# Performance work log

Measured on AMD Instinct MI355X. Metric: run time of the kernel, lower is better.

The kernel has to match this reference:

```python
import jax, jax.numpy as jnp
import numpy as np

D_MODEL = 1024
N_HEAD = 16
B, T = 4, 2048


def setup_inputs() -> dict:
    key = jax.random.key(0)
    k1, k2, k3, k4, k5 = jax.random.split(key, 5)
    s = 0.02
    return {
        "x": jax.random.normal(k1, (B, T, D_MODEL), dtype=jnp.float32),
        "w_attn": jax.random.normal(k2, (3 * D_MODEL, D_MODEL), dtype=jnp.float32) * s,
        "b_attn": jax.random.normal(k3, (3 * D_MODEL,), dtype=jnp.float32) * s,
        "w_proj": jax.random.normal(k4, (D_MODEL, D_MODEL), dtype=jnp.float32) * s,
        "b_proj": jax.random.normal(k5, (D_MODEL,), dtype=jnp.float32) * s,
    }


def reference(x, w_attn, b_attn, w_proj, b_proj):
    # x: [B, T, C]
    Bb, Tt, C = x.shape
    H = N_HEAD
    dk = C // H
    scale = 1.0 / np.sqrt(dk).astype(np.float32)

    qkv = x @ w_attn.T + b_attn                      # [B, T, 3C]
    q, k, v = jnp.split(qkv, 3, axis=-1)             # each [B, T, C]
    # -> [B, H, T, dk]
    q = q.reshape(Bb, Tt, H, dk).transpose(0, 2, 1, 3)
    k = k.reshape(Bb, Tt, H, dk).transpose(0, 2, 1, 3)
    v = v.reshape(Bb, Tt, H, dk).transpose(0, 2, 1, 3)

    att = jnp.einsum("bhqd,bhkd->bhqk", q, k) * scale   # [B, H, T, T]
    att = jax.nn.softmax(att, axis=-1)
    y = jnp.einsum("bhqk,bhkd->bhqd", att, v)            # [B, H, T, dk]
    y = y.transpose(0, 2, 1, 3).reshape(Bb, Tt, C)       # [B, T, C]
    return y @ w_proj.T + b_proj
```

## Files before the change

kernel.cpp:

```cpp
#include <hip/hip_runtime.h>
#include <hip/hip_bf16.h>

typedef __attribute__((ext_vector_type(8))) short short8;
typedef __attribute__((ext_vector_type(4))) short short4v;
typedef __attribute__((ext_vector_type(4))) float floatx4;
typedef __attribute__((ext_vector_type(16))) float floatx16;

#define B_ 4
#define T_ 2048
#define C_ 1024
#define H_ 16
#define DK_ 64
#define M_ (B_ * T_)
#define N3_ (3 * C_)

#define QSCALE 0.1803368801111243f

__device__ __forceinline__ unsigned short f2bf(float f) {
    union { float f; unsigned u; } v; v.f = f;
    unsigned r = v.u + 0x7fffu + ((v.u >> 16) & 1u);
    return (unsigned short)(r >> 16);
}
__device__ __forceinline__ unsigned fbits(float f) {
    union { float f; unsigned u; } v; v.f = f; return v.u;
}
__device__ __forceinline__ unsigned pack_bf16(float a, float b) {
#if __has_builtin(__builtin_amdgcn_cvt_pk_bf16_f32)
    typedef __attribute__((ext_vector_type(2))) __bf16 bf16x2;
    bf16x2 r = __builtin_amdgcn_cvt_pk_bf16_f32(a, b);
    union { bf16x2 v; unsigned u; } c; c.v = r; return c.u;
#else
    return __builtin_amdgcn_perm(fbits(b) + 0x8000u, fbits(a) + 0x8000u, 0x07060302u);
#endif
}

__device__ __forceinline__ void gload_lds16(const unsigned short* g, unsigned short* l) {
    __builtin_amdgcn_global_load_lds(
        (const __attribute__((address_space(1))) unsigned int*)(const void*)g,
        (__attribute__((address_space(3))) unsigned int*)(void*)l, 16, 0, 0);
}

#define NX4 (M_ * C_ / 4)
#define NA4 (N3_ * C_ / 4)
#define NP4 (C_ * C_ / 4)
__global__ __launch_bounds__(256) void cast3_kernel(const float* __restrict__ x,
                                                    const float* __restrict__ wa,
                                                    const float* __restrict__ wp,
                                                    unsigned short* __restrict__ xb,
                                                    unsigned short* __restrict__ wab,
                                                    unsigned short* __restrict__ wpb) {
    int i = blockIdx.x * 256 + threadIdx.x;
    const float* src; unsigned short* dst; int j;
    if (i < NX4) { src = x; dst = xb; j = i; }
    else if (i < NX4 + NA4) { src = wa; dst = wab; j = i - NX4; }
    else { src = wp; dst = wpb; j = i - NX4 - NA4; }
    float4 v = ((const float4*)src)[j];
    ushort4 o;
    o.x = f2bf(v.x); o.y = f2bf(v.y); o.z = f2bf(v.z); o.w = f2bf(v.w);
    ((ushort4*)dst)[j] = o;
}

#define BM 128
#define BN 128
#define BK 32

__global__ __launch_bounds__(256) void gemm_qkv(const unsigned short* __restrict__ A,
                                                const unsigned short* __restrict__ W,
                                                const float* __restrict__ bias,
                                                unsigned short* __restrict__ qout,
                                                unsigned short* __restrict__ kout,
                                                unsigned short* __restrict__ vout) {
    const int Kd = C_;
    __shared__ unsigned short As[BM * BK];
    __shared__ unsigned short Bs[BN * BK];
    int lin = blockIdx.y * gridDim.x + blockIdx.x;
    int cpx = (gridDim.x * gridDim.y) >> 3;
    int swz = (lin & 7) * cpx + (lin >> 3);
    int m0 = (swz / gridDim.x) * BM;
    int n0 = (swz % gridDim.x) * BN;
    int tid = threadIdx.x;
    int lane = tid & 63, w = tid >> 6;
    int wm = (w >> 1) * 64, wn = (w & 1) * 64;
    int l16 = lane & 15, quad = lane >> 4;
    int r4 = lane >> 2, c4 = (lane & 3) * 8;

    floatx4 acc[4][4] = {};
    for (int kt = 0; kt < Kd; kt += BK) {
        __syncthreads();
        for (int t = 0; t < 2; ++t) {
            int rbase = w * 32 + t * 16;
            gload_lds16(&A[(size_t)(m0 + rbase + r4) * Kd + kt + c4], &As[rbase * BK]);
            gload_lds16(&W[(size_t)(n0 + rbase + r4) * Kd + kt + c4], &Bs[rbase * BK]);
        }
        __syncthreads();
        short8 af[4], bf[4];
        for (int i = 0; i < 4; ++i)
            af[i] = *(const short8*)&As[(wm + 16 * i + l16) * BK + quad * 8];
        for (int j = 0; j < 4; ++j)
            bf[j] = *(const short8*)&Bs[(wn + 16 * j + l16) * BK + quad * 8];
        for (int i = 0; i < 4; ++i)
            for (int j = 0; j < 4; ++j)
                acc[i][j] = __builtin_amdgcn_mfma_f32_16x16x32_bf16(af[i], bf[j], acc[i][j], 0, 0, 0);
    }
    for (int i = 0; i < 4; ++i)
        for (int j = 0; j < 4; ++j) {
            int col = n0 + wn + 16 * j + l16;
            float bval = bias[col];
            int sec = col >> 10, cc = col & 1023;
            int h = cc >> 6, d = cc & 63;
            float qs = (sec == 0) ? QSCALE : 1.0f;
            unsigned short* dst = (sec == 0) ? qout : ((sec == 1) ? kout : vout);
            for (int r = 0; r < 4; ++r) {
                int m = m0 + wm + 16 * i + quad * 4 + r;
                int b = m >> 11, t = m & (T_ - 1);
                int bh = b * H_ + h;
                dst[((size_t)bh * T_ + t) * DK_ + d] = f2bf((acc[i][j][r] + bval) * qs);
            }
        }
}

__global__ __launch_bounds__(256) void gemm_proj(const unsigned short* __restrict__ A,
                                                 const unsigned short* __restrict__ W,
                                                 const float* __restrict__ bias,
                                                 float* __restrict__ out) {
    const int Kd = C_;
    __shared__ unsigned short As[BM * BK];
    __shared__ unsigned short Bs[BN * BK];
    int lin = blockIdx.y * gridDim.x + blockIdx.x;
    int cpx = (gridDim.x * gridDim.y) >> 3;
    int swz = (lin & 7) * cpx + (lin >> 3);
    int m0 = (swz / gridDim.x) * BM;
    int n0 = (swz % gridDim.x) * BN;
    int tid = threadIdx.x;
    int lane = tid & 63, w = tid >> 6;
    int wm = (w >> 1) * 64, wn = (w & 1) * 64;
    int l16 = lane & 15, quad = lane >> 4;
    int r4 = lane >> 2, c4 = (lane & 3) * 8;

    floatx4 acc[4][4] = {};
    for (int kt = 0; kt < Kd; kt += BK) {
        __syncthreads();
        for (int t = 0; t < 2; ++t) {
            int rbase = w * 32 + t * 16;
            gload_lds16(&A[(size_t)(m0 + rbase + r4) * Kd + kt + c4], &As[rbase * BK]);
            gload_lds16(&W[(size_t)(n0 + rbase + r4) * Kd + kt + c4], &Bs[rbase * BK]);
        }
        __syncthreads();
        short8 af[4], bf[4];
        for (int i = 0; i < 4; ++i)
            af[i] = *(const short8*)&As[(wm + 16 * i + l16) * BK + quad * 8];
        for (int j = 0; j < 4; ++j)
            bf[j] = *(const short8*)&Bs[(wn + 16 * j + l16) * BK + quad * 8];
        for (int i = 0; i < 4; ++i)
            for (int j = 0; j < 4; ++j)
                acc[i][j] = __builtin_amdgcn_mfma_f32_16x16x32_bf16(af[i], bf[j], acc[i][j], 0, 0, 0);
    }
    for (int i = 0; i < 4; ++i)
        for (int j = 0; j < 4; ++j) {
            int col = n0 + wn + 16 * j + l16;
            float bval = bias[col];
            for (int r = 0; r < 4; ++r) {
                int m = m0 + wm + 16 * i + quad * 4 + r;
                out[(size_t)m * C_ + col] = acc[i][j][r] + bval;
            }
        }
}

#define TLD 258
__global__ __launch_bounds__(256) void vtrans_kernel(const unsigned short* __restrict__ V,
                                                     unsigned short* __restrict__ Vt) {
    __shared__ unsigned short L[64 * TLD];
    int bid = blockIdx.x;
    int t0 = (bid & 7) * 256;
    int bh = bid >> 3;
    int tid = threadIdx.x;
    const unsigned short* src = V + ((size_t)bh * T_ + t0) * DK_;
    unsigned short* dst = Vt + (size_t)bh * DK_ * T_ + t0;
    for (int it = 0; it < 8; ++it) {
        int t = it * 32 + (tid >> 3);
        int dseg = (tid & 7) * 8;
        short8 v = *(const short8*)&src[(size_t)t * DK_ + dseg];
        for (int j = 0; j < 8; ++j)
            L[(dseg + j) * TLD + t] = ((unsigned short*)&v)[j];
    }
    __syncthreads();
    for (int it = 0; it < 8; ++it) {
        int d = it * 8 + (tid >> 5);
        int toff = (tid & 31) * 8;
        short8 r = *(const short8*)&L[d * TLD + toff];
        *(short8*)&dst[(size_t)d * T_ + toff] = r;
    }
}

#define KT 64
#define LD 72

__global__ __launch_bounds__(256, 2) void attn_kernel(const unsigned short* __restrict__ Q,
                                                      const unsigned short* __restrict__ Kv,
                                                      const unsigned short* __restrict__ Vt,
                                                      unsigned short* __restrict__ Y) {
    __shared__ unsigned short smem[128 * LD];
    unsigned short* Ks = smem;
    unsigned short* Vts = smem + 64 * LD;

    int bid = blockIdx.x;
    int qt = bid & 7;
    int bh = bid >> 3;
    int b = bh >> 4, hh = bh & 15;
    const unsigned short* qh = Q + (size_t)bh * T_ * DK_;
    const unsigned short* kh = Kv + (size_t)bh * T_ * DK_;
    const unsigned short* vtg = Vt + (size_t)bh * DK_ * T_;

    int tid = threadIdx.x, lane = tid & 63, w = tid >> 6;
    int l31 = lane & 31, h = lane >> 5;
    int qrA = qt * 256 + w * 32;
    int qrB = qrA + 128;

    short8 qfA[4], qfB[4];
    for (int c = 0; c < 4; ++c) {
        qfA[c] = *(const short8*)&qh[(size_t)(qrA + l31) * DK_ + 16 * c + 8 * h];
        qfB[c] = *(const short8*)&qh[(size_t)(qrB + l31) * DK_ + 16 * c + 8 * h];
    }

    floatx16 oA0 = {}, oA1 = {}, oB0 = {}, oB1 = {};
    float lA = 0.f, lB = 0.f;

    for (int kt = 0; kt < T_; kt += KT) {
        __syncthreads();
        for (int it = 0; it < 2; ++it) {
            int idx = tid + it * 256;
            int r8 = idx >> 3, c8 = (idx & 7) * 8;
            *(short8*)&Ks[r8 * LD + c8] = *(const short8*)&kh[(size_t)(kt + r8) * DK_ + c8];
            int vd = r8 * LD + (c8 & 48) + ((c8 & 8) >> 1);
            union { short8 s; short4v q[2]; } u;
            u.s = *(const short8*)&vtg[(size_t)r8 * T_ + kt + c8];
            *(short4v*)&Vts[vd] = u.q[0];
            *(short4v*)&Vts[vd + 8] = u.q[1];
        }
        __syncthreads();

        floatx16 sA0 = {}, sA1 = {}, sB0 = {}, sB1 = {};
        for (int c = 0; c < 4; ++c) {
            short8 kf0 = *(const short8*)&Ks[l31 * LD + 16 * c + 8 * h];
            short8 kf1 = *(const short8*)&Ks[(32 + l31) * LD + 16 * c + 8 * h];
            sA0 = __builtin_amdgcn_mfma_f32_32x32x16_bf16(kf0, qfA[c], sA0, 0, 0, 0);
            sA1 = __builtin_amdgcn_mfma_f32_32x32x16_bf16(kf1, qfA[c], sA1, 0, 0, 0);
            sB0 = __builtin_amdgcn_mfma_f32_32x32x16_bf16(kf0, qfB[c], sB0, 0, 0, 0);
            sB1 = __builtin_amdgcn_mfma_f32_32x32x16_bf16(kf1, qfB[c], sB1, 0, 0, 0);
        }

        unsigned pA[16], pB[16];
        float tsA = 0.f, tsB = 0.f;
        for (int r2 = 0; r2 < 8; ++r2) {
            float a0 = __builtin_amdgcn_exp2f(sA0[2 * r2]);
            float a1 = __builtin_amdgcn_exp2f(sA0[2 * r2 + 1]);
            tsA += a0 + a1; pA[r2] = pack_bf16(a0, a1);
            float a2 = __builtin_amdgcn_exp2f(sA1[2 * r2]);
            float a3 = __builtin_amdgcn_exp2f(sA1[2 * r2 + 1]);
            tsA += a2 + a3; pA[8 + r2] = pack_bf16(a2, a3);
            float b0 = __builtin_amdgcn_exp2f(sB0[2 * r2]);
            float b1 = __builtin_amdgcn_exp2f(sB0[2 * r2 + 1]);
            tsB += b0 + b1; pB[r2] = pack_bf16(b0, b1);
            float b2 = __builtin_amdgcn_exp2f(sB1[2 * r2]);
            float b3 = __builtin_amdgcn_exp2f(sB1[2 * r2 + 1]);
            tsB += b2 + b3; pB[8 + r2] = pack_bf16(b2, b3);
        }
        lA += tsA; lB += tsB;

        for (int c = 0; c < 4; ++c) {
            short8 vf0 = *(const short8*)&Vts[l31 * LD + 16 * c + 8 * h];
            short8 vf1 = *(const short8*)&Vts[(32 + l31) * LD + 16 * c + 8 * h];
            union { unsigned u[4]; short8 s; } fA, fB;
            for (int j = 0; j < 4; ++j) { fA.u[j] = pA[4 * c + j]; fB.u[j] = pB[4 * c + j]; }
            oA0 = __builtin_amdgcn_mfma_f32_32x32x16_bf16(vf0, fA.s, oA0, 0, 0, 0);
            oA1 = __builtin_amdgcn_mfma_f32_32x32x16_bf16(vf1, fA.s, oA1, 0, 0, 0);
            oB0 = __builtin_amdgcn_mfma_f32_32x32x16_bf16(vf0, fB.s, oB0, 0, 0, 0);
            oB1 = __builtin_amdgcn_mfma_f32_32x32x16_bf16(vf1, fB.s, oB1, 0, 0, 0);
        }
    }

    float invA = 1.0f / (lA + __shfl_xor(lA, 32, 64));
    float invB = 1.0f / (lB + __shfl_xor(lB, 32, 64));
    int q_l = tid >> 1, seg = tid & 1;

    __syncthreads();
    for (int a = 0; a < 4; ++a) {
        ushort4 u;
        u.x = f2bf(oA0[4 * a + 0] * invA); u.y = f2bf(oA0[4 * a + 1] * invA);
        u.z = f2bf(oA0[4 * a + 2] * invA); u.w = f2bf(oA0[4 * a + 3] * invA);
        *(ushort4*)&smem[(w * 32 + l31) * LD + 8 * a + 4 * h] = u;
        ushort4 v;
        v.x = f2bf(oA1[4 * a + 0] * invA); v.y = f2bf(oA1[4 * a + 1] * invA);
        v.z = f2bf(oA1[4 * a + 2] * invA); v.w = f2bf(oA1[4 * a + 3] * invA);
        *(ushort4*)&smem[(w * 32 + l31) * LD + 32 + 8 * a + 4 * h] = v;
    }
    __syncthreads();
    {
        const unsigned short* srcp = &smem[(size_t)q_l * LD + seg * 32];
        unsigned short* dstp = &Y[((size_t)b * T_ + qt * 256 + q_l) * C_ + hh * DK_ + seg * 32];
        for (int j = 0; j < 4; ++j)
            *(short8*)&dstp[8 * j] = *(const short8*)&srcp[8 * j];
    }
    __syncthreads();
    for (int a = 0; a < 4; ++a) {
        ushort4 u;
        u.x = f2bf(oB0[4 * a + 0] * invB); u.y = f2bf(oB0[4 * a + 1] * invB);
        u.z = f2bf(oB0[4 * a + 2] * invB); u.w = f2bf(oB0[4 * a + 3] * invB);
        *(ushort4*)&smem[(w * 32 + l31) * LD + 8 * a + 4 * h] = u;
        ushort4 v;
        v.x = f2bf(oB1[4 * a + 0] * invB); v.y = f2bf(oB1[4 * a + 1] * invB);
        v.z = f2bf(oB1[4 * a + 2] * invB); v.w = f2bf(oB1[4 * a + 3] * invB);
        *(ushort4*)&smem[(w * 32 + l31) * LD + 32 + 8 * a + 4 * h] = v;
    }
    __syncthreads();
    {
        const unsigned short* srcp = &smem[(size_t)q_l * LD + seg * 32];
        unsigned short* dstp = &Y[((size_t)b * T_ + qt * 256 + 128 + q_l) * C_ + hh * DK_ + seg * 32];
        for (int j = 0; j < 4; ++j)
            *(short8*)&dstp[8 * j] = *(const short8*)&srcp[8 * j];
    }
}

extern "C" void kernel_launch(void* const* d_in, const int* in_sizes, int n_in,
                              void* d_out, int out_size, void* d_ws, size_t ws_size,
                              hipStream_t stream) {
    const float* x      = (const float*)d_in[0];
    const float* w_attn = (const float*)d_in[1];
    const float* b_attn = (const float*)d_in[2];
    const float* w_proj = (const float*)d_in[3];
    const float* b_proj = (const float*)d_in[4];
    float* out = (float*)d_out;

    unsigned short* ws = (unsigned short*)d_ws;
    unsigned short* xb  = ws;
    unsigned short* wab = xb  + (size_t)M_ * C_;
    unsigned short* wpb = wab + (size_t)N3_ * C_;
    unsigned short* qb  = wpb + (size_t)C_ * C_;
    unsigned short* kb  = qb  + (size_t)M_ * C_;
    unsigned short* vb  = kb  + (size_t)M_ * C_;
    unsigned short* yb  = vb  + (size_t)M_ * C_;
    unsigned short* vtb = xb;

    cast3_kernel<<<(NX4 + NA4 + NP4) / 256, 256, 0, stream>>>(x, w_attn, w_proj, xb, wab, wpb);
    gemm_qkv<<<dim3(N3_ / BN, M_ / BM), 256, 0, stream>>>(xb, wab, b_attn, qb, kb, vb);
    vtrans_kernel<<<B_ * H_ * (T_ / 256), 256, 0, stream>>>(vb, vtb);
    attn_kernel<<<B_ * H_ * (T_ / 256), 256, 0, stream>>>(qb, kb, vtb, yb);
    gemm_proj<<<dim3(C_ / BN, M_ / BM), 256, 0, stream>>>(yb, wpb, b_proj, out);
}
```

Measured before the change: 272.4 us.

## Replace QKV GEMM with 256x256 pipelined 8-wave kernel and fuse V transpose

Replaces the simple 128x128 QKV GEMM with a 256x256, 8-wave kernel. It double-buffers 64-wide K slices in LDS with an XOR swizzle and interleaves global-to-LDS staging with MFMA phases, using barriers and s_setprio. The epilogue writes V directly in transposed [bh][d][t] layout, which removes the separate transpose kernel and its extra pass over memory. The cost is heavy LDS use (128KB per block) and hand-tuned waitcnt logic that is fragile and could race if the counts are wrong.

```diff
diff --git a/kernel.cpp b/kernel.cpp
--- a/kernel.cpp
+++ b/kernel.cpp
@@ -60,64 +60,180 @@
     ((ushort4*)dst)[j] = o;
 }
 
+#define QBM 256
+#define QBN 256
+#define QBK 64
+#define QNT (C_ / QBK)
+
+__device__ __forceinline__ void stage_half(const unsigned short* g, unsigned short* ldst,
+                                           int w, int srow, int scol) {
+    for (int i = 0; i < 2; ++i) {
+        int s = i * 8 + w;
+        gload_lds16(g + (size_t)(s * 8 + srow) * C_ + scol, ldst + s * 512);
+    }
+}
+
+__global__ __launch_bounds__(512, 2) void gemm_qkv8(const unsigned short* __restrict__ A,
+                                                    const unsigned short* __restrict__ W,
+                                                    const float* __restrict__ bias,
+                                                    unsigned short* __restrict__ qout,
+                                                    unsigned short* __restrict__ kout,
+                                                    unsigned short* __restrict__ vout) {
+    __shared__ unsigned short Lds[2][2][QBM * QBK];
+
+    int lin = blockIdx.y * gridDim.x + blockIdx.x;
+    int cpx = (gridDim.x * gridDim.y) >> 3;
+    int swzb = (lin & 7) * cpx + (lin >> 3);
+    int m0 = (swzb / gridDim.x) * QBM;
+    int n0 = (swzb % gridDim.x) * QBN;
+
+    int tid = threadIdx.x, lane = tid & 63, w = tid >> 6;
+    int wr = w >> 2, wc = w & 3;
+    int l16 = lane & 15, quad = lane >> 4;
+
+    int srow = lane >> 3;
+    int scol = ((lane & 7) ^ srow) * 8;
+    int rswz = (l16 & 7) << 3;
+    int c0 = (quad * 8) ^ rswz;
+
+    floatx4 acc[8][4] = {};
+    short8 af[4][2], bf[4][2];
+
+    const unsigned short* Ag = A + (size_t)m0 * C_;
+    const unsigned short* Wg = W + (size_t)n0 * C_;
+
+    stage_half(Ag, &Lds[0][0][0], w, srow, scol);
+    stage_half(Ag + (size_t)128 * C_, &Lds[0][0][8192], w, srow, scol);
+    stage_half(Wg, &Lds[0][1][0], w, srow, scol);
+    stage_half(Wg + (size_t)128 * C_, &Lds[0][1][8192], w, srow, scol);
+    stage_half(Wg + QBK, &Lds[1][1][0], w, srow, scol);
+    stage_half(Wg + (size_t)128 * C_ + QBK, &Lds[1][1][8192], w, srow, scol);
+    asm volatile("s_waitcnt vmcnt(4)" ::: "memory");
+    __builtin_amdgcn_s_barrier();
+
+#pragma unroll 1
+    for (int t = 0; t < QNT; ++t) {
+        int cur = t & 1;
+        const unsigned short* Ab = &Lds[cur][0][0];
+        const unsigned short* Bb = &Lds[cur][1][0];
+
+#pragma unroll
+        for (int m = 0; m < 4; ++m) {
+            int r = wr * 128 + m * 16 + l16;
+            af[m][0] = *(const short8*)&Ab[r * 64 + c0];
+            af[m][1] = *(const short8*)&Ab[r * 64 + (c0 ^ 32)];
+        }
+#pragma unroll
+        for (int nf = 0; nf < 2; ++nf) {
+            int r = wc * 64 + nf * 16 + l16;
+            bf[nf][0] = *(const short8*)&Bb[r * 64 + c0];
+            bf[nf][1] = *(const short8*)&Bb[r * 64 + (c0 ^ 32)];
+        }
+        if (t + 1 < QNT)
+            stage_half(Ag + (size_t)(t + 1) * QBK, &Lds[cur ^ 1][0][0], w, srow, scol);
+        asm volatile("s_waitcnt lgkmcnt(8)" ::: "memory");
+        __builtin_amdgcn_s_barrier();
+        asm volatile("s_waitcnt lgkmcnt(0)" ::: "memory");
+        __builtin_amdgcn_s_setprio(1);
+#pragma unroll
+        for (int m = 0; m < 4; ++m)
+#pragma unroll
+            for (int n = 0; n < 2; ++n) {
+                acc[m][n] = __builtin_amdgcn_mfma_f32_16x16x32_bf16(af[m][0], bf[n][0], acc[m][n], 0, 0, 0);
+                acc[m][n] = __builtin_amdgcn_mfma_f32_16x16x32_bf16(af[m][1], bf[n][1], acc[m][n], 0, 0, 0);
+            }
+        __builtin_amdgcn_s_setprio(0);
+        __builtin_amdgcn_s_barrier();
+
+#pragma unroll
+        for (int nf = 2; nf < 4; ++nf) {
+            int r = wc * 64 + nf * 16 + l16;
+            bf[nf][0] = *(const short8*)&Bb[r * 64 + c0];
+            bf[nf][1] = *(const short8*)&Bb[r * 64 + (c0 ^ 32)];
+        }
+        if (t + 1 < QNT)
+            stage_half(Ag + (size_t)128 * C_ + (t + 1) * QBK, &Lds[cur ^ 1][0][8192], w, srow, scol);
+        __builtin_amdgcn_s_barrier();
+        asm volatile("s_waitcnt lgkmcnt(0)" ::: "memory");
+        __builtin_amdgcn_s_setprio(1);
+#pragma unroll
+        for (int m = 0; m < 4; ++m)
+#pragma unroll
+            for (int n = 2; n < 4; ++n) {
+                acc[m][n] = __builtin_amdgcn_mfma_f32_16x16x32_bf16(af[m][0], bf[n][0], acc[m][n], 0, 0, 0);
+                acc[m][n] = __builtin_amdgcn_mfma_f32_16x16x32_bf16(af[m][1], bf[n][1], acc[m][n], 0, 0, 0);
+            }
+        __builtin_amdgcn_s_setprio(0);
+        __builtin_amdgcn_s_barrier();
+
+#pragma unroll
+        for (int m = 0; m < 4; ++m) {
+            int r = wr * 128 + 64 + m * 16 + l16;
+            af[m][0] = *(const short8*)&Ab[r * 64 + c0];
+            af[m][1] = *(const short8*)&Ab[r * 64 + (c0 ^ 32)];
+        }
+        if (t + 2 < QNT)
+            stage_half(Wg + (size_t)(t + 2) * QBK, &Lds[cur][1][0], w, srow, scol);
+        __builtin_amdgcn_s_barrier();
+        asm volatile("s_waitcnt lgkmcnt(0)" ::: "memory");
+        __builtin_amdgcn_s_setprio(1);
+#pragma unroll
+        for (int m = 0; m < 4; ++m)
+#pragma unroll
+            for (int n = 0; n < 2; ++n) {
+                acc[4 + m][n] = __builtin_amdgcn_mfma_f32_16x16x32_bf16(af[m][0], bf[n][0], acc[4 + m][n], 0, 0, 0);
+                acc[4 + m][n] = __builtin_amdgcn_mfma_f32_16x16x32_bf16(af[m][1], bf[n][1], acc[4 + m][n], 0, 0, 0);
+            }
+        __builtin_amdgcn_s_setprio(0);
+        __builtin_amdgcn_s_barrier();
+
+        if (t + 2 < QNT)
+            stage_half(Wg + (size_t)128 * C_ + (t + 2) * QBK, &Lds[cur][1][8192], w, srow, scol);
+        if (t >= QNT - 2) asm volatile("s_waitcnt vmcnt(0)" ::: "memory");
+        else              asm volatile("s_waitcnt vmcnt(4)" ::: "memory");
+        __builtin_amdgcn_s_barrier();
+        __builtin_amdgcn_s_setprio(1);
+#pragma unroll
+        for (int m = 0; m < 4; ++m)
+#pragma unroll
+            for (int n = 2; n < 4; ++n) {
+                acc[4 + m][n] = __builtin_amdgcn_mfma_f32_16x16x32_bf16(af[m][0], bf[n][0], acc[4 + m][n], 0, 0, 0);
+                acc[4 + m][n] = __builtin_amdgcn_mfma_f32_16x16x32_bf16(af[m][1], bf[n][1], acc[4 + m][n], 0, 0, 0);
+            }
+        __builtin_amdgcn_s_setprio(0);
+        __builtin_amdgcn_s_barrier();
+    }
+
+#pragma unroll
+    for (int mf = 0; mf < 8; ++mf)
+#pragma unroll
+        for (int nf = 0; nf < 4; ++nf) {
+            int col = n0 + wc * 64 + nf * 16 + l16;
+            float bval = bias[col];
+            int sec = col >> 10, cc = col & 1023;
+            int hh = cc >> 6, d = cc & 63;
+            int mbase = m0 + wr * 128 + mf * 16 + quad * 4;
+            int b = mbase >> 11, tt = mbase & (T_ - 1);
+            int bh = b * H_ + hh;
+            if (sec == 2) {
+                ushort4 o;
+                o.x = f2bf(acc[mf][nf][0] + bval);
+                o.y = f2bf(acc[mf][nf][1] + bval);
+                o.z = f2bf(acc[mf][nf][2] + bval);
+                o.w = f2bf(acc[mf][nf][3] + bval);
+                *(ushort4*)&vout[((size_t)bh * DK_ + d) * T_ + tt] = o;
+            } else {
+                float qs = (sec == 0) ? QSCALE : 1.0f;
+                unsigned short* dst = (sec == 0) ? qout : kout;
+                for (int r = 0; r < 4; ++r)
+                    dst[((size_t)bh * T_ + tt + r) * DK_ + d] = f2bf((acc[mf][nf][r] + bval) * qs);
+            }
+        }
+}
+
 #define BM 128
 #define BN 128
 #define BK 32
-
-__global__ __launch_bounds__(256) void gemm_qkv(const unsigned short* __restrict__ A,
-                                                const unsigned short* __restrict__ W,
-                                                const float* __restrict__ bias,
-                                                unsigned short* __restrict__ qout,
-                                                unsigned short* __restrict__ kout,
-                                                unsigned short* __restrict__ vout) {
-    const int Kd = C_;
-    __shared__ unsigned short As[BM * BK];
-    __shared__ unsigned short Bs[BN * BK];
-    int lin = blockIdx.y * gridDim.x + blockIdx.x;
-    int cpx = (gridDim.x * gridDim.y) >> 3;
-    int swz = (lin & 7) * cpx + (lin >> 3);
-    int m0 = (swz / gridDim.x) * BM;
-    int n0 = (swz % gridDim.x) * BN;
-    int tid = threadIdx.x;
-    int lane = tid & 63, w = tid >> 6;
-    int wm = (w >> 1) * 64, wn = (w & 1) * 64;
-    int l16 = lane & 15, quad = lane >> 4;
-    int r4 = lane >> 2, c4 = (lane & 3) * 8;
-
-    floatx4 acc[4][4] = {};
-    for (int kt = 0; kt < Kd; kt += BK) {
-        __syncthreads();
-        for (int t = 0; t < 2; ++t) {
-            int rbase = w * 32 + t * 16;
-            gload_lds16(&A[(size_t)(m0 + rbase + r4) * Kd + kt + c4], &As[rbase * BK]);
-            gload_lds16(&W[(size_t)(n0 + rbase + r4) * Kd + kt + c4], &Bs[rbase * BK]);
-        }
-        __syncthreads();
-        short8 af[4], bf[4];
-        for (int i = 0; i < 4; ++i)
-            af[i] = *(const short8*)&As[(wm + 16 * i + l16) * BK + quad * 8];
-        for (int j = 0; j < 4; ++j)
-            bf[j] = *(const short8*)&Bs[(wn + 16 * j + l16) * BK + quad * 8];
-        for (int i = 0; i < 4; ++i)
-            for (int j = 0; j < 4; ++j)
-                acc[i][j] = __builtin_amdgcn_mfma_f32_16x16x32_bf16(af[i], bf[j], acc[i][j], 0, 0, 0);
-    }
-    for (int i = 0; i < 4; ++i)
-        for (int j = 0; j < 4; ++j) {
-            int col = n0 + wn + 16 * j + l16;
-            float bval = bias[col];
-            int sec = col >> 10, cc = col & 1023;
-            int h = cc >> 6, d = cc & 63;
-            float qs = (sec == 0) ? QSCALE : 1.0f;
-            unsigned short* dst = (sec == 0) ? qout : ((sec == 1) ? kout : vout);
-            for (int r = 0; r < 4; ++r) {
-                int m = m0 + wm + 16 * i + quad * 4 + r;
-                int b = m >> 11, t = m & (T_ - 1);
-                int bh = b * H_ + h;
-                dst[((size_t)bh * T_ + t) * DK_ + d] = f2bf((acc[i][j][r] + bval) * qs);
-            }
-        }
-}
 
 __global__ __launch_bounds__(256) void gemm_proj(const unsigned short* __restrict__ A,
                                                  const unsigned short* __restrict__ W,
@@ -166,32 +282,6 @@
         }
 }
 
-#define TLD 258
-__global__ __launch_bounds__(256) void vtrans_kernel(const unsigned short* __restrict__ V,
-                                                     unsigned short* __restrict__ Vt) {
-    __shared__ unsigned short L[64 * TLD];
-    int bid = blockIdx.x;
-    int t0 = (bid & 7) * 256;
-    int bh = bid >> 3;
-    int tid = threadIdx.x;
-    const unsigned short* src = V + ((size_t)bh * T_ + t0) * DK_;
-    unsigned short* dst = Vt + (size_t)bh * DK_ * T_ + t0;
-    for (int it = 0; it < 8; ++it) {
-        int t = it * 32 + (tid >> 3);
-        int dseg = (tid & 7) * 8;
-        short8 v = *(const short8*)&src[(size_t)t * DK_ + dseg];
-        for (int j = 0; j < 8; ++j)
-            L[(dseg + j) * TLD + t] = ((unsigned short*)&v)[j];
-    }
-    __syncthreads();
-    for (int it = 0; it < 8; ++it) {
-        int d = it * 8 + (tid >> 5);
-        int toff = (tid & 31) * 8;
-        short8 r = *(const short8*)&L[d * TLD + toff];
-        *(short8*)&dst[(size_t)d * T_ + toff] = r;
-    }
-}
-
 #define KT 64
 #define LD 72
 
@@ -339,11 +429,9 @@
     unsigned short* kb  = qb  + (size_t)M_ * C_;
     unsigned short* vb  = kb  + (size_t)M_ * C_;
     unsigned short* yb  = vb  + (size_t)M_ * C_;
-    unsigned short* vtb = xb;
 
     cast3_kernel<<<(NX4 + NA4 + NP4) / 256, 256, 0, stream>>>(x, w_attn, w_proj, xb, wab, wpb);
-    gemm_qkv<<<dim3(N3_ / BN, M_ / BM), 256, 0, stream>>>(xb, wab, b_attn, qb, kb, vb);
-    vtrans_kernel<<<B_ * H_ * (T_ / 256), 256, 0, stream>>>(vb, vtb);
-    attn_kernel<<<B_ * H_ * (T_ / 256), 256, 0, stream>>>(qb, kb, vtb, yb);
+    gemm_qkv8<<<dim3(N3_ / QBN, M_ / QBM), 512, 0, stream>>>(xb, wab, b_attn, qb, kb, vb);
+    attn_kernel<<<B_ * H_ * (T_ / 256), 256, 0, stream>>>(qb, kb, vb, yb);
     gemm_proj<<<dim3(C_ / BN, M_ / BM), 256, 0, stream>>>(yb, wpb, b_proj, out);
 }
```

Measured after the change: 267.3 us. No clear change (-1.9%).

## Fuse V transpose into QKV GEMM epilogue and reorder attention block mapping

Applied to the files above, without the earlier changes.

The QKV GEMM epilogue now writes V directly in transposed [bh, d, t] layout using 4-wide vector stores, which removes the separate vtrans kernel launch and its extra read/write pass over V. The attention kernel's block index mapping is also changed so consecutive blocks cover different heads rather than different query tiles of the same head. This changes how K/V reuse shows up in L2 across concurrently running blocks. The transposed V stores in the GEMM epilogue are strided across d, which may be less coalesced than the old row-major writes.

```diff
diff --git a/kernel.cpp b/kernel.cpp
--- a/kernel.cpp
+++ b/kernel.cpp
@@ -108,13 +108,21 @@
             float bval = bias[col];
             int sec = col >> 10, cc = col & 1023;
             int h = cc >> 6, d = cc & 63;
-            float qs = (sec == 0) ? QSCALE : 1.0f;
-            unsigned short* dst = (sec == 0) ? qout : ((sec == 1) ? kout : vout);
-            for (int r = 0; r < 4; ++r) {
-                int m = m0 + wm + 16 * i + quad * 4 + r;
-                int b = m >> 11, t = m & (T_ - 1);
-                int bh = b * H_ + h;
-                dst[((size_t)bh * T_ + t) * DK_ + d] = f2bf((acc[i][j][r] + bval) * qs);
+            int m = m0 + wm + 16 * i + quad * 4;
+            int b = m >> 11, t = m & (T_ - 1);
+            int bh = b * H_ + h;
+            if (sec == 2) {
+                ushort4 o;
+                o.x = f2bf(acc[i][j][0] + bval);
+                o.y = f2bf(acc[i][j][1] + bval);
+                o.z = f2bf(acc[i][j][2] + bval);
+                o.w = f2bf(acc[i][j][3] + bval);
+                *(ushort4*)&vout[((size_t)bh * DK_ + d) * T_ + t] = o;
+            } else {
+                float qs = (sec == 0) ? QSCALE : 1.0f;
+                unsigned short* dst = (sec == 0) ? qout : kout;
+                for (int r = 0; r < 4; ++r)
+                    dst[((size_t)bh * T_ + t + r) * DK_ + d] = f2bf((acc[i][j][r] + bval) * qs);
             }
         }
 }
@@ -166,32 +174,6 @@
         }
 }
 
-#define TLD 258
-__global__ __launch_bounds__(256) void vtrans_kernel(const unsigned short* __restrict__ V,
-                                                     unsigned short* __restrict__ Vt) {
-    __shared__ unsigned short L[64 * TLD];
-    int bid = blockIdx.x;
-    int t0 = (bid & 7) * 256;
-    int bh = bid >> 3;
-    int tid = threadIdx.x;
-    const unsigned short* src = V + ((size_t)bh * T_ + t0) * DK_;
-    unsigned short* dst = Vt + (size_t)bh * DK_ * T_ + t0;
-    for (int it = 0; it < 8; ++it) {
-        int t = it * 32 + (tid >> 3);
-        int dseg = (tid & 7) * 8;
-        short8 v = *(const short8*)&src[(size_t)t * DK_ + dseg];
-        for (int j = 0; j < 8; ++j)
-            L[(dseg + j) * TLD + t] = ((unsigned short*)&v)[j];
-    }
-    __syncthreads();
-    for (int it = 0; it < 8; ++it) {
-        int d = it * 8 + (tid >> 5);
-        int toff = (tid & 31) * 8;
-        short8 r = *(const short8*)&L[d * TLD + toff];
-        *(short8*)&dst[(size_t)d * T_ + toff] = r;
-    }
-}
-
 #define KT 64
 #define LD 72
 
@@ -204,8 +186,8 @@
     unsigned short* Vts = smem + 64 * LD;
 
     int bid = blockIdx.x;
-    int qt = bid & 7;
-    int bh = bid >> 3;
+    int qt = bid >> 6;
+    int bh = bid & 63;
     int b = bh >> 4, hh = bh & 15;
     const unsigned short* qh = Q + (size_t)bh * T_ * DK_;
     const unsigned short* kh = Kv + (size_t)bh * T_ * DK_;
@@ -339,11 +321,9 @@
     unsigned short* kb  = qb  + (size_t)M_ * C_;
     unsigned short* vb  = kb  + (size_t)M_ * C_;
     unsigned short* yb  = vb  + (size_t)M_ * C_;
-    unsigned short* vtb = xb;
 
     cast3_kernel<<<(NX4 + NA4 + NP4) / 256, 256, 0, stream>>>(x, w_attn, w_proj, xb, wab, wpb);
     gemm_qkv<<<dim3(N3_ / BN, M_ / BM), 256, 0, stream>>>(xb, wab, b_attn, qb, kb, vb);
-    vtrans_kernel<<<B_ * H_ * (T_ / 256), 256, 0, stream>>>(vb, vtb);
-    attn_kernel<<<B_ * H_ * (T_ / 256), 256, 0, stream>>>(qb, kb, vtb, yb);
+    attn_kernel<<<B_ * H_ * (T_ / 256), 256, 0, stream>>>(qb, kb, vb, yb);
     gemm_proj<<<dim3(C_ / BN, M_ / BM), 256, 0, stream>>>(yb, wpb, b_proj, out);
 }
```

Result: slower. 279.9 us (+2.8%).
